# Optimization experiments

Hardware: AMD Instinct MI355X
Metric: run time of the kernel (lower is better)

## Reference

```python
import jax, jax.numpy as jnp
import numpy as np

N_NODES = 100000
N_EDGES = 1600000
NEG_SLOPE = 0.2  # PyG GATConv default


def _glorot(key, shape):
    fan = sum(shape[:2]) if len(shape) > 1 else shape[0] * 2
    s = jnp.sqrt(6.0 / fan)
    return jax.random.uniform(key, shape, jnp.float32, -s, s)


def gat_layer(x, src, dst, edge_attr, W, a_src, a_dst, We, a_e, b, heads, out_ch, concat):
    """Faithful PyG GATConv (add_self_loops=True, fill_value='mean', edge_dim set)."""
    n = x.shape[0]
    # self-loop edge_attr = mean of incoming edge_attr per dst node (0 if none)
    deg = jax.ops.segment_sum(jnp.ones((src.shape[0],), edge_attr.dtype), dst, num_segments=n)
    loop_attr = jax.ops.segment_sum(edge_attr, dst, num_segments=n) / jnp.maximum(deg, 1.0)[:, None]
    loop = jnp.arange(n, dtype=src.dtype)
    src_f = jnp.concatenate([src, loop])
    dst_f = jnp.concatenate([dst, loop])
    ea = jnp.concatenate([edge_attr, loop_attr], axis=0)
    # node transform -> [n, H, C]
    h = (x @ W).reshape(n, heads, out_ch)
    al_src = jnp.sum(h * a_src, axis=-1)  # [n, H]
    al_dst = jnp.sum(h * a_dst, axis=-1)  # [n, H]
    e = (ea @ We).reshape(-1, heads, out_ch)
    al_e = jnp.sum(e * a_e, axis=-1)      # [Ef, H]
    alpha = jax.nn.leaky_relu(al_src[src_f] + al_dst[dst_f] + al_e, negative_slope=NEG_SLOPE)
    # segment softmax over destination nodes (every node has a self loop)
    m = jax.ops.segment_max(alpha, dst_f, num_segments=n)
    ex = jnp.exp(alpha - m[dst_f])
    den = jax.ops.segment_sum(ex, dst_f, num_segments=n)
    att = ex / den[dst_f]                 # [Ef, H]
    out = jax.ops.segment_sum(att[:, :, None] * h[src_f], dst_f, num_segments=n)  # [n, H, C]
    out = out.reshape(n, heads * out_ch) if concat else out.mean(axis=1)
    return out + b


def setup_inputs() -> dict:
    key = jax.random.key(0)
    ks = jax.random.split(key, 20)
    x = jax.random.normal(ks[0], (N_NODES, 5), jnp.float32)
    edge_index = jax.random.randint(ks[1], (2, N_EDGES), 0, N_NODES, jnp.int64)
    edge_attr = jax.random.normal(ks[2], (N_EDGES, 2), jnp.float32)
    # conv1: in=5, out=32, heads=4, concat -> 128
    p = {
        "W1": _glorot(ks[3], (5, 128)), "aS1": _glorot(ks[4], (4, 32)),
        "aD1": _glorot(ks[5], (4, 32)), "We1": _glorot(ks[6], (2, 128)),
        "aE1": _glorot(ks[7], (4, 32)), "b1": jnp.zeros((128,), jnp.float32),
        # conv2: in=128, out=32, heads=2, concat -> 64
        "W2": _glorot(ks[8], (128, 64)), "aS2": _glorot(ks[9], (2, 32)),
        "aD2": _glorot(ks[10], (2, 32)), "We2": _glorot(ks[11], (2, 64)),
        "aE2": _glorot(ks[12], (2, 32)), "b2": jnp.zeros((64,), jnp.float32),
        # conv3: in=64, out=1, heads=1, concat=False
        "W3": _glorot(ks[13], (64, 1)), "aS3": _glorot(ks[14], (1, 1)),
        "aD3": _glorot(ks[15], (1, 1)), "We3": _glorot(ks[16], (2, 1)),
        "aE3": _glorot(ks[17], (1, 1)), "b3": jnp.zeros((1,), jnp.float32),
    }
    return {"x": x, "edge_index": edge_index, "edge_attr": edge_attr, **p}


def reference(x, edge_index, edge_attr,
              W1, aS1, aD1, We1, aE1, b1,
              W2, aS2, aD2, We2, aE2, b2,
              W3, aS3, aD3, We3, aE3, b3):
    src, dst = edge_index[0], edge_index[1]
    h = gat_layer(x, src, dst, edge_attr, W1, aS1, aD1, We1, aE1, b1, 4, 32, True)
    h = jax.nn.elu(h)  # dropout is identity in eval
    h = gat_layer(h, src, dst, edge_attr, W2, aS2, aD2, We2, aE2, b2, 2, 32, True)
    h = jax.nn.elu(h)
    h = gat_layer(h, src, dst, edge_attr, W3, aS3, aD3, We3, aE3, b3, 1, 1, False)
    return jax.nn.sigmoid(h).squeeze(-1)  # [N]
```

## Files before the change

### kernel.cpp

```cpp
#include <hip/hip_runtime.h>
#include <math.h>

#define NN 100000
#define NE 1600000
#define NPB 256
#define NB 391
#define NCHUNK 256
#define CH ((NE + NCHUNK - 1) / NCHUNK)
#define LOG2E 1.44269504088896f

__device__ __forceinline__ float lrelu(float x) { return fmaxf(x, 0.2f * x); }
__device__ __forceinline__ float elu1(float x) { return x > 0.f ? x : (__expf(x) - 1.f); }
__device__ __forceinline__ float fexp2(float x) {
#if __has_builtin(__builtin_amdgcn_exp2f)
    return __builtin_amdgcn_exp2f(x);
#else
    return exp2f(x);
#endif
}
__device__ __forceinline__ unsigned bf16rne(float f) {
    unsigned u = __float_as_uint(f);
    return (u + 0x7FFFu + ((u >> 16) & 1u)) >> 16;
}
__device__ __forceinline__ float bf16lo(unsigned u) { return __uint_as_float(u << 16); }
__device__ __forceinline__ float bf16hi(unsigned u) {
    return __uint_as_float(u & 0xFFFF0000u);
}

__global__ void __launch_bounds__(256) k_binA0(const int* __restrict__ dst,
                                               int* __restrict__ bucket_cnt) {
    __shared__ int hist[NB];
    int t = threadIdx.x;
    for (int b = t; b < NB; b += 256) hist[b] = 0;
    __syncthreads();
    int c0 = blockIdx.x * CH, c1 = min(NE, c0 + CH);
    for (int e = c0 + t; e < c1; e += 256) atomicAdd(&hist[dst[e] >> 8], 1);
    __syncthreads();
    for (int b = t; b < NB; b += 256)
        if (hist[b]) atomicAdd(&bucket_cnt[b], hist[b]);
}

__global__ void k_bscan(const int* __restrict__ bucket_cnt, int* __restrict__ bucket_base,
                        int* __restrict__ bucket_tail) {
    __shared__ int s[512];
    int t = threadIdx.x;
    int v = (t < NB) ? bucket_cnt[t] : 0;
    s[t] = v;
    __syncthreads();
    for (int off = 1; off < 512; off <<= 1) {
        int x = (t >= off) ? s[t - off] : 0;
        __syncthreads();
        if (t >= off) s[t] += x;
        __syncthreads();
    }
    if (t < NB) {
        int ex = s[t] - v;
        bucket_base[t] = ex;
        bucket_tail[t] = ex;
        if (t == NB - 1) bucket_base[NB] = s[t];
    }
}

__global__ void __launch_bounds__(256) k_binA2(const int* __restrict__ src,
                                               const int* __restrict__ dst,
                                               const float* __restrict__ ea,
                                               int* __restrict__ bucket_tail,
                                               uint2* __restrict__ binned,
                                               unsigned char* __restrict__ dstb) {
    __shared__ int hist[NB], base_l[NB], cursor[NB];
    int t = threadIdx.x;
    for (int b = t; b < NB; b += 256) {
        hist[b] = 0;
        cursor[b] = 0;
    }
    __syncthreads();
    int c0 = blockIdx.x * CH, c1 = min(NE, c0 + CH);
    for (int e = c0 + t; e < c1; e += 256) atomicAdd(&hist[dst[e] >> 8], 1);
    __syncthreads();
    for (int b = t; b < NB; b += 256)
        if (hist[b]) base_l[b] = atomicAdd(&bucket_tail[b], hist[b]);
    __syncthreads();
    for (int e = c0 + t; e < c1; e += 256) {
        int d = dst[e];
        int bkt = d >> 8;
        int idx = atomicAdd(&cursor[bkt], 1);
        int pos = base_l[bkt] + idx;
        unsigned pk = bf16rne(ea[2 * e]) | (bf16rne(ea[2 * e + 1]) << 16);
        binned[pos] = make_uint2((unsigned)src[e], pk);
        dstb[pos] = (unsigned char)(d & 255);
    }
}

__global__ void __launch_bounds__(256) k_binB(const int* __restrict__ bucket_base,
                                              const uint2* __restrict__ binned,
                                              const unsigned char* __restrict__ dstb,
                                              int* __restrict__ rowptr,
                                              uint2* __restrict__ edges) {
    __shared__ int hist[NPB], pre[NPB], cursor[NPB];
    int b = blockIdx.x, t = threadIdx.x;
    int bb = bucket_base[b], be = bucket_base[b + 1];
    int nb0 = b << 8;
    hist[t] = 0;
    __syncthreads();
    for (int e = bb + t; e < be; e += 256) atomicAdd(&hist[dstb[e]], 1);
    __syncthreads();
    int v = hist[t];
    pre[t] = v;
    __syncthreads();
    for (int off = 1; off < 256; off <<= 1) {
        int x = (t >= off) ? pre[t - off] : 0;
        __syncthreads();
        if (t >= off) pre[t] += x;
        __syncthreads();
    }
    int ex = pre[t] - v;
    if (nb0 + t <= NN) rowptr[nb0 + t] = bb + ex;
    cursor[t] = bb + ex;
    __syncthreads();
    for (int e = bb + t; e < be; e += 256) {
        uint2 rec = binned[e];
        int pos = atomicAdd(&cursor[dstb[e]], 1);
        edges[pos] = rec;
    }
}

__global__ void k_la(const int* __restrict__ rowptr, const uint2* __restrict__ edges,
                     float* __restrict__ la) {
    int n = (blockIdx.x * blockDim.x + threadIdx.x) >> 6;
    if (n >= NN) return;
    int lane = threadIdx.x & 63;
    int s0 = rowptr[n], e0 = rowptr[n + 1];
    float a0 = 0.f, a1 = 0.f;
    for (int e = s0 + lane; e < e0; e += 64) {
        unsigned pk = edges[e].y;
        a0 += bf16lo(pk);
        a1 += bf16hi(pk);
    }
#pragma unroll
    for (int off = 32; off > 0; off >>= 1) {
        a0 += __shfl_xor(a0, off);
        a1 += __shfl_xor(a1, off);
    }
    if (lane == 0) {
        float d = fmaxf((float)(e0 - s0), 1.0f);
        la[2 * n] = a0 / d;
        la[2 * n + 1] = a1 / d;
    }
}

template <int H, int C>
__global__ void k_me(const float* __restrict__ We, const float* __restrict__ aE,
                     float* __restrict__ me) {
    int t = threadIdx.x;
    if (t >= 2 * H) return;
    int d = t / H, hd = t % H;
    float s = 0.f;
    for (int c = 0; c < C; c++) s += We[d * H * C + hd * C + c] * aE[hd * C + c];
    me[t] = s * LOG2E;
}

__global__ void k_vsd(const float* __restrict__ W1, const float* __restrict__ aS1,
                      const float* __restrict__ aD1, float* __restrict__ vsd) {
    int t = threadIdx.x;
    if (t >= 40) return;
    const float* a = (t < 20) ? aS1 : aD1;
    int r = t % 20, hd = r / 5, i = r % 5;
    float s = 0.f;
    for (int c = 0; c < 32; c++) s += W1[i * 128 + hd * 32 + c] * a[hd * 32 + c];
    vsd[t] = s * LOG2E;
}

__global__ void k_prep1(const float* __restrict__ x, const float* __restrict__ vsd,
                        float4* __restrict__ xp, float4* __restrict__ als1,
                        float4* __restrict__ ald1) {
    int n = blockIdx.x * blockDim.x + threadIdx.x;
    if (n >= NN) return;
    float x0 = x[5 * n], x1 = x[5 * n + 1], x2 = x[5 * n + 2], x3 = x[5 * n + 3],
          x4 = x[5 * n + 4];
    xp[2 * n] = make_float4(x0, x1, x2, x3);
    xp[2 * n + 1] = make_float4(x4, 0.f, 0.f, 0.f);
    float sv[4], dv[4];
#pragma unroll
    for (int hd = 0; hd < 4; hd++) {
        const float* vS = vsd + hd * 5;
        const float* vD = vsd + 20 + hd * 5;
        sv[hd] = x0 * vS[0] + x1 * vS[1] + x2 * vS[2] + x3 * vS[3] + x4 * vS[4];
        dv[hd] = x0 * vD[0] + x1 * vD[1] + x2 * vD[2] + x3 * vD[3] + x4 * vD[4];
    }
    als1[n] = make_float4(sv[0], sv[1], sv[2], sv[3]);
    ald1[n] = make_float4(dv[0], dv[1], dv[2], dv[3]);
}

__global__ void k_agg1(const int* __restrict__ rowptr, const uint2* __restrict__ edges,
                       const float4* __restrict__ xp, const float* __restrict__ als1,
                       const float* __restrict__ ald1, const float* __restrict__ la,
                       const float* __restrict__ me, float* __restrict__ xw) {
    int t = blockIdx.x * blockDim.x + threadIdx.x;
    if (t >= NN * 4) return;
    int n = t >> 2, hd = t & 3;
    float me0 = me[hd], me1 = me[4 + hd];
    float aldn = ald1[t];
    float aself = lrelu(als1[t] + aldn + la[2 * n] * me0 + la[2 * n + 1] * me1);
    int start = rowptr[n], end = rowptr[n + 1];
    float den = 1.f;
    float4 xa = xp[2 * n];
    float xb = xp[2 * n + 1].x;
    float a0 = xa.x, a1 = xa.y, a2 = xa.z, a3 = xa.w, a4 = xb;
    for (int e = start; e < end; ++e) {
        uint2 ep = edges[e];
        int s = (int)ep.x;
        float a = lrelu(als1[s * 4 + hd] + aldn + bf16lo(ep.y) * me0 + bf16hi(ep.y) * me1);
        float p = fexp2(a - aself);
        den += p;
        float4 sa = xp[2 * s];
        float sb = xp[2 * s + 1].x;
        a0 += p * sa.x;
        a1 += p * sa.y;
        a2 += p * sa.z;
        a3 += p * sa.w;
        a4 += p * sb;
    }
    float r = 1.f / den;
    float* w = xw + (size_t)n * 20 + hd * 5;
    w[0] = a0 * r;
    w[1] = a1 * r;
    w[2] = a2 * r;
    w[3] = a3 * r;
    w[4] = a4 * r;
}

__global__ void __launch_bounds__(256) k_l2trans(
        const float* __restrict__ xw, const float* __restrict__ W1,
        const float* __restrict__ b1, const float* __restrict__ W2,
        const float* __restrict__ aS2, const float* __restrict__ aD2,
        unsigned short* __restrict__ h2q, float* __restrict__ als2,
        float* __restrict__ ald2) {
    __shared__ float sx[64 * 132];
    int nb = blockIdx.x * 64, t = threadIdx.x;
    {
        int nl = t >> 2, q = t & 3;
        int node = nb + nl;
        float w[20];
        if (node < NN) {
#pragma unroll
            for (int i = 0; i < 20; i++) w[i] = xw[(size_t)node * 20 + i];
        } else {
#pragma unroll
            for (int i = 0; i < 20; i++) w[i] = 0.f;
        }
#pragma unroll
        for (int k = 0; k < 32; k++) {
            int ch = q + 4 * k;
            int hd = ch >> 5;
            float v = w[hd * 5] * W1[ch] + w[hd * 5 + 1] * W1[128 + ch] +
                      w[hd * 5 + 2] * W1[256 + ch] + w[hd * 5 + 3] * W1[384 + ch] +
                      w[hd * 5 + 4] * W1[512 + ch] + b1[ch];
            sx[nl * 132 + ch] = (node < NN) ? elu1(v) : 0.f;
        }
    }
    __syncthreads();
    int jq = t & 15, ng = t >> 4;
    int j4 = jq * 4;
    float4 acc[4];
#pragma unroll
    for (int p = 0; p < 4; p++) acc[p] = make_float4(0.f, 0.f, 0.f, 0.f);
    for (int ic = 0; ic < 128; ic += 4) {
        float4 s[4];
#pragma unroll
        for (int p = 0; p < 4; p++)
            s[p] = *(const float4*)(sx + (ng * 4 + p) * 132 + ic);
#pragma unroll
        for (int r = 0; r < 4; r++) {
            float4 wv = *(const float4*)(W2 + (ic + r) * 64 + j4);
#pragma unroll
            for (int p = 0; p < 4; p++) {
                float sv = (r == 0) ? s[p].x : (r == 1) ? s[p].y : (r == 2) ? s[p].z : s[p].w;
                acc[p].x += sv * wv.x;
                acc[p].y += sv * wv.y;
                acc[p].z += sv * wv.z;
                acc[p].w += sv * wv.w;
            }
        }
    }
    int hd = jq >> 3;
    float4 a_s = *(const float4*)(aS2 + j4);
    float4 a_d = *(const float4*)(aD2 + j4);
    float pS[4], pD[4];
#pragma unroll
    for (int p = 0; p < 4; p++) {
        pS[p] = acc[p].x * a_s.x + acc[p].y * a_s.y + acc[p].z * a_s.z + acc[p].w * a_s.w;
        pD[p] = acc[p].x * a_d.x + acc[p].y * a_d.y + acc[p].z * a_d.z + acc[p].w * a_d.w;
    }
#pragma unroll
    for (int off = 1; off < 8; off <<= 1) {
#pragma unroll
        for (int p = 0; p < 4; p++) {
            pS[p] += __shfl_xor(pS[p], off);
            pD[p] += __shfl_xor(pD[p], off);
        }
    }
#pragma unroll
    for (int p = 0; p < 4; p++) {
        int node = nb + ng * 4 + p;
        if (node < NN) {
            ushort4 q;
            q.x = (unsigned short)bf16rne(acc[p].x);
            q.y = (unsigned short)bf16rne(acc[p].y);
            q.z = (unsigned short)bf16rne(acc[p].z);
            q.w = (unsigned short)bf16rne(acc[p].w);
            *(ushort4*)(h2q + (size_t)node * 64 + j4) = q;
            if ((jq & 7) == 0) {
                als2[node * 2 + hd] = pS[p] * LOG2E;
                ald2[node * 2 + hd] = pD[p] * LOG2E;
            }
        }
    }
}

__global__ void k_agg2(const int* __restrict__ rowptr, const uint2* __restrict__ edges,
                       const unsigned short* __restrict__ h2q,
                       const float* __restrict__ als2, const float* __restrict__ ald2,
                       const float* __restrict__ la, const float* __restrict__ me,
                       const float* __restrict__ b2, const float* __restrict__ W3,
                       float* __restrict__ h3) {
    int t = blockIdx.x * blockDim.x + threadIdx.x;
    if (t >= NN * 4) return;
    int n = t >> 2, sub = t & 3, hd = sub >> 1, qh = sub & 1;
    int cbase = hd * 32 + qh * 16;
    float me0 = me[hd], me1 = me[2 + hd];
    float aldn = ald2[n * 2 + hd];
    float aself = lrelu(als2[n * 2 + hd] + aldn + la[2 * n] * me0 + la[2 * n + 1] * me1);
    int start = rowptr[n], end = rowptr[n + 1];
    float den = 1.f;
    float acc[16];
    {
        const uint4* hp = (const uint4*)(h2q + (size_t)n * 64 + cbase);
        uint4 u0 = hp[0], u1 = hp[1];
        acc[0] = bf16lo(u0.x); acc[1] = bf16hi(u0.x);
        acc[2] = bf16lo(u0.y); acc[3] = bf16hi(u0.y);
        acc[4] = bf16lo(u0.z); acc[5] = bf16hi(u0.z);
        acc[6] = bf16lo(u0.w); acc[7] = bf16hi(u0.w);
        acc[8] = bf16lo(u1.x); acc[9] = bf16hi(u1.x);
        acc[10] = bf16lo(u1.y); acc[11] = bf16hi(u1.y);
        acc[12] = bf16lo(u1.z); acc[13] = bf16hi(u1.z);
        acc[14] = bf16lo(u1.w); acc[15] = bf16hi(u1.w);
    }
    for (int e = start; e < end; ++e) {
        uint2 ep = edges[e];
        int s = (int)ep.x;
        float a = lrelu(als2[s * 2 + hd] + aldn + bf16lo(ep.y) * me0 + bf16hi(ep.y) * me1);
        float p = fexp2(a - aself);
        den += p;
        const uint4* sp = (const uint4*)(h2q + (size_t)s * 64 + cbase);
        uint4 u0 = sp[0], u1 = sp[1];
        acc[0] += p * bf16lo(u0.x); acc[1] += p * bf16hi(u0.x);
        acc[2] += p * bf16lo(u0.y); acc[3] += p * bf16hi(u0.y);
        acc[4] += p * bf16lo(u0.z); acc[5] += p * bf16hi(u0.z);
        acc[6] += p * bf16lo(u0.w); acc[7] += p * bf16hi(u0.w);
        acc[8] += p * bf16lo(u1.x); acc[9] += p * bf16hi(u1.x);
        acc[10] += p * bf16lo(u1.y); acc[11] += p * bf16hi(u1.y);
        acc[12] += p * bf16lo(u1.z); acc[13] += p * bf16hi(u1.z);
        acc[14] += p * bf16lo(u1.w); acc[15] += p * bf16hi(u1.w);
    }
    float r = 1.f / den;
    float part = 0.f;
#pragma unroll
    for (int c = 0; c < 16; c++) {
        float v = elu1(acc[c] * r + b2[cbase + c]);
        part += v * W3[cbase + c];
    }
    part += __shfl_xor(part, 1);
    part += __shfl_xor(part, 2);
    if (sub == 0) h3[n] = part;
}

__global__ void k_agg3(const int* __restrict__ rowptr, const uint2* __restrict__ edges,
                       const float* __restrict__ h, const float* __restrict__ aS3,
                       const float* __restrict__ aD3, const float* __restrict__ la,
                       const float* __restrict__ me, const float* __restrict__ b,
                       float* __restrict__ out) {
    int n = (blockIdx.x * blockDim.x + threadIdx.x) >> 6;
    if (n >= NN) return;
    int lane = threadIdx.x & 63;
    float me0 = me[0], me1 = me[1];
    float aSs = aS3[0] * LOG2E, aDs = aD3[0] * LOG2E;
    float hn = h[n];
    float ald_n = hn * aDs;
    float aself = lrelu(hn * aSs + ald_n + la[2 * n] * me0 + la[2 * n + 1] * me1);
    int start = rowptr[n], end = rowptr[n + 1];
    float den = 0.f, num = 0.f;
    for (int e = start + lane; e < end; e += 64) {
        uint2 ep = edges[e];
        int s = (int)ep.x;
        float hv = h[s];
        float a = lrelu(hv * aSs + ald_n + bf16lo(ep.y) * me0 + bf16hi(ep.y) * me1);
        float p = fexp2(a - aself);
        den += p;
        num += p * hv;
    }
#pragma unroll
    for (int off = 32; off > 0; off >>= 1) {
        den += __shfl_xor(den, off);
        num += __shfl_xor(num, off);
    }
    if (lane == 0) {
        den += 1.f;
        num += hn;
        float v = num / den + b[0];
        out[n] = 1.f / (1.f + __expf(-v));
    }
}

extern "C" void kernel_launch(void* const* d_in, const int* in_sizes, int n_in,
                              void* d_out, int out_size, void* d_ws, size_t ws_size,
                              hipStream_t stream) {
    const float* x   = (const float*)d_in[0];
    const int*   ei  = (const int*)d_in[1];
    const float* ea  = (const float*)d_in[2];
    const float* W1  = (const float*)d_in[3];
    const float* aS1 = (const float*)d_in[4];
    const float* aD1 = (const float*)d_in[5];
    const float* We1 = (const float*)d_in[6];
    const float* aE1 = (const float*)d_in[7];
    const float* b1  = (const float*)d_in[8];
    const float* W2  = (const float*)d_in[9];
    const float* aS2 = (const float*)d_in[10];
    const float* aD2 = (const float*)d_in[11];
    const float* We2 = (const float*)d_in[12];
    const float* aE2 = (const float*)d_in[13];
    const float* b2  = (const float*)d_in[14];
    const float* W3  = (const float*)d_in[15];
    const float* aS3 = (const float*)d_in[16];
    const float* aD3 = (const float*)d_in[17];
    const float* We3 = (const float*)d_in[18];
    const float* aE3 = (const float*)d_in[19];
    const float* b3  = (const float*)d_in[20];

    const int* srcv = ei;
    const int* dstv = ei + NE;

    char* basep = (char*)d_ws;
    size_t off = 0;
    auto alloc = [&](size_t nbytes) -> void* {
        void* p = basep + off;
        off += (nbytes + 255) & ~(size_t)255;
        return p;
    };
    int*    bucket_cnt  = (int*)alloc((size_t)(NB + 1) * 4);
    int*    bucket_base = (int*)alloc((size_t)(NB + 1) * 4);
    int*    bucket_tail = (int*)alloc((size_t)(NB + 1) * 4);
    int*    rowptr      = (int*)alloc((size_t)(NN + 1) * 4);
    uint2*  binned      = (uint2*)alloc((size_t)NE * 8);
    unsigned char* dstb = (unsigned char*)alloc((size_t)NE);
    uint2*  edges       = (uint2*)alloc((size_t)NE * 8);
    float*  la          = (float*)alloc((size_t)NN * 8);
    float*  me          = (float*)alloc(256);
    float*  vsd         = (float*)alloc(256);
    float4* xp          = (float4*)alloc((size_t)NN * 32);
    float4* als1        = (float4*)alloc((size_t)NN * 16);
    float4* ald1        = (float4*)alloc((size_t)NN * 16);
    float*  xw          = (float*)alloc((size_t)NN * 80);
    unsigned short* h2q = (unsigned short*)alloc((size_t)NN * 128);
    float*  als2        = (float*)alloc((size_t)NN * 8);
    float*  ald2        = (float*)alloc((size_t)NN * 8);
    float*  h3          = (float*)alloc((size_t)NN * 4);
    (void)ws_size; (void)in_sizes; (void)n_in; (void)out_size;

    auto cdiv = [](long long a, long long b) { return (int)((a + b - 1) / b); };
    const int BS = 256;

    hipMemsetAsync(bucket_cnt, 0, (size_t)(NB + 1) * 4, stream);
    k_binA0<<<NCHUNK, 256, 0, stream>>>(dstv, bucket_cnt);
    k_bscan<<<1, 512, 0, stream>>>(bucket_cnt, bucket_base, bucket_tail);
    k_binA2<<<NCHUNK, 256, 0, stream>>>(srcv, dstv, ea, bucket_tail, binned, dstb);
    k_binB<<<NB, 256, 0, stream>>>(bucket_base, binned, dstb, rowptr, edges);
    k_la<<<cdiv(NN, 4), 256, 0, stream>>>(rowptr, edges, la);

    k_me<4, 32><<<1, 64, 0, stream>>>(We1, aE1, me);
    k_vsd<<<1, 64, 0, stream>>>(W1, aS1, aD1, vsd);
    k_prep1<<<cdiv(NN, BS), BS, 0, stream>>>(x, vsd, xp, als1, ald1);
    k_agg1<<<cdiv((long long)NN * 4, BS), BS, 0, stream>>>(rowptr, edges, xp,
                                                           (const float*)als1,
                                                           (const float*)ald1, la, me, xw);

    k_l2trans<<<cdiv(NN, 64), 256, 0, stream>>>(xw, W1, b1, W2, aS2, aD2, h2q, als2, ald2);
    k_me<2, 32><<<1, 64, 0, stream>>>(We2, aE2, me);
    k_agg2<<<cdiv((long long)NN * 4, BS), BS, 0, stream>>>(rowptr, edges, h2q, als2, ald2,
                                                           la, me, b2, W3, h3);

    k_me<1, 1><<<1, 64, 0, stream>>>(We3, aE3, me);
    k_agg3<<<cdiv(NN, 4), 256, 0, stream>>>(rowptr, edges, h3, aS3, aD3, la, me,
                                            b3, (float*)d_out);
}
```

Before: 360.6 us.

## Fuse self-loop attr mean into binning, merge constant kernels, shrink l2trans tile

The per-node mean of incoming edge attributes is now accumulated with shared-memory float atomics inside the bucket scatter kernel, which removes the separate k_la pass over the edge array. The four tiny constant-precompute kernels are merged into one launch that writes into a single buffer, cutting launch count. The layer-2 transform block now handles 32 nodes instead of 64, doubling the grid and halving shared memory and registers per block to raise occupancy. The price is shared float atomic contention in binB and a changed accumulation order for the mean.

```diff
diff --git a/kernel.cpp b/kernel.cpp
--- a/kernel.cpp
+++ b/kernel.cpp
@@ -95,12 +95,16 @@
                                               const uint2* __restrict__ binned,
                                               const unsigned char* __restrict__ dstb,
                                               int* __restrict__ rowptr,
-                                              uint2* __restrict__ edges) {
+                                              uint2* __restrict__ edges,
+                                              float* __restrict__ la) {
     __shared__ int hist[NPB], pre[NPB], cursor[NPB];
+    __shared__ float ea0s[NPB], ea1s[NPB];
     int b = blockIdx.x, t = threadIdx.x;
     int bb = bucket_base[b], be = bucket_base[b + 1];
     int nb0 = b << 8;
     hist[t] = 0;
+    ea0s[t] = 0.f;
+    ea1s[t] = 0.f;
     __syncthreads();
     for (int e = bb + t; e < be; e += 256) atomicAdd(&hist[dstb[e]], 1);
     __syncthreads();
@@ -119,55 +123,46 @@
     __syncthreads();
     for (int e = bb + t; e < be; e += 256) {
         uint2 rec = binned[e];
-        int pos = atomicAdd(&cursor[dstb[e]], 1);
+        unsigned char d = dstb[e];
+        int pos = atomicAdd(&cursor[d], 1);
         edges[pos] = rec;
-    }
-}
-
-__global__ void k_la(const int* __restrict__ rowptr, const uint2* __restrict__ edges,
-                     float* __restrict__ la) {
-    int n = (blockIdx.x * blockDim.x + threadIdx.x) >> 6;
-    if (n >= NN) return;
-    int lane = threadIdx.x & 63;
-    int s0 = rowptr[n], e0 = rowptr[n + 1];
-    float a0 = 0.f, a1 = 0.f;
-    for (int e = s0 + lane; e < e0; e += 64) {
-        unsigned pk = edges[e].y;
-        a0 += bf16lo(pk);
-        a1 += bf16hi(pk);
-    }
-#pragma unroll
-    for (int off = 32; off > 0; off >>= 1) {
-        a0 += __shfl_xor(a0, off);
-        a1 += __shfl_xor(a1, off);
-    }
-    if (lane == 0) {
-        float d = fmaxf((float)(e0 - s0), 1.0f);
-        la[2 * n] = a0 / d;
-        la[2 * n + 1] = a1 / d;
-    }
-}
-
-template <int H, int C>
-__global__ void k_me(const float* __restrict__ We, const float* __restrict__ aE,
-                     float* __restrict__ me) {
+        atomicAdd(&ea0s[d], bf16lo(rec.y));
+        atomicAdd(&ea1s[d], bf16hi(rec.y));
+    }
+    __syncthreads();
+    int n = nb0 + t;
+    if (n < NN) {
+        float dg = fmaxf((float)v, 1.0f);
+        la[2 * n] = ea0s[t] / dg;
+        la[2 * n + 1] = ea1s[t] / dg;
+    }
+}
+
+__global__ void k_const(const float* __restrict__ We1, const float* __restrict__ aE1,
+                        const float* __restrict__ We2, const float* __restrict__ aE2,
+                        const float* __restrict__ We3, const float* __restrict__ aE3,
+                        const float* __restrict__ W1, const float* __restrict__ aS1,
+                        const float* __restrict__ aD1, float* __restrict__ cbuf) {
     int t = threadIdx.x;
-    if (t >= 2 * H) return;
-    int d = t / H, hd = t % H;
-    float s = 0.f;
-    for (int c = 0; c < C; c++) s += We[d * H * C + hd * C + c] * aE[hd * C + c];
-    me[t] = s * LOG2E;
-}
-
-__global__ void k_vsd(const float* __restrict__ W1, const float* __restrict__ aS1,
-                      const float* __restrict__ aD1, float* __restrict__ vsd) {
-    int t = threadIdx.x;
-    if (t >= 40) return;
-    const float* a = (t < 20) ? aS1 : aD1;
-    int r = t % 20, hd = r / 5, i = r % 5;
-    float s = 0.f;
-    for (int c = 0; c < 32; c++) s += W1[i * 128 + hd * 32 + c] * a[hd * 32 + c];
-    vsd[t] = s * LOG2E;
+    if (t < 8) {
+        int d = t >> 2, hd = t & 3;
+        float s = 0.f;
+        for (int c = 0; c < 32; c++) s += We1[d * 128 + hd * 32 + c] * aE1[hd * 32 + c];
+        cbuf[t] = s * LOG2E;
+    } else if (t < 12) {
+        int idx = t - 8, d = idx >> 1, hd = idx & 1;
+        float s = 0.f;
+        for (int c = 0; c < 32; c++) s += We2[d * 64 + hd * 32 + c] * aE2[hd * 32 + c];
+        cbuf[t] = s * LOG2E;
+    } else if (t < 14) {
+        cbuf[t] = We3[t - 12] * aE3[0] * LOG2E;
+    } else if (t >= 16 && t < 56) {
+        int r = (t - 16) % 20, hd = r / 5, i = r % 5;
+        const float* a = (t - 16 < 20) ? aS1 : aD1;
+        float s = 0.f;
+        for (int c = 0; c < 32; c++) s += W1[i * 128 + hd * 32 + c] * a[hd * 32 + c];
+        cbuf[t] = s * LOG2E;
+    }
 }
 
 __global__ void k_prep1(const float* __restrict__ x, const float* __restrict__ vsd,
@@ -235,10 +230,10 @@
         const float* __restrict__ aS2, const float* __restrict__ aD2,
         unsigned short* __restrict__ h2q, float* __restrict__ als2,
         float* __restrict__ ald2) {
-    __shared__ float sx[64 * 132];
-    int nb = blockIdx.x * 64, t = threadIdx.x;
+    __shared__ float sx[32 * 132];
+    int nb = blockIdx.x * 32, t = threadIdx.x;
     {
-        int nl = t >> 2, q = t & 3;
+        int nl = t >> 3, q = t & 7;
         int node = nb + nl;
         float w[20];
         if (node < NN) {
@@ -249,8 +244,8 @@
             for (int i = 0; i < 20; i++) w[i] = 0.f;
         }
 #pragma unroll
-        for (int k = 0; k < 32; k++) {
-            int ch = q + 4 * k;
+        for (int k = 0; k < 16; k++) {
+            int ch = q + 8 * k;
             int hd = ch >> 5;
             float v = w[hd * 5] * W1[ch] + w[hd * 5 + 1] * W1[128 + ch] +
                       w[hd * 5 + 2] * W1[256 + ch] + w[hd * 5 + 3] * W1[384 + ch] +
@@ -261,19 +256,19 @@
     __syncthreads();
     int jq = t & 15, ng = t >> 4;
     int j4 = jq * 4;
-    float4 acc[4];
-#pragma unroll
-    for (int p = 0; p < 4; p++) acc[p] = make_float4(0.f, 0.f, 0.f, 0.f);
+    float4 acc[2];
+#pragma unroll
+    for (int p = 0; p < 2; p++) acc[p] = make_float4(0.f, 0.f, 0.f, 0.f);
     for (int ic = 0; ic < 128; ic += 4) {
-        float4 s[4];
-#pragma unroll
-        for (int p = 0; p < 4; p++)
-            s[p] = *(const float4*)(sx + (ng * 4 + p) * 132 + ic);
+        float4 s[2];
+#pragma unroll
+        for (int p = 0; p < 2; p++)
+            s[p] = *(const float4*)(sx + (ng * 2 + p) * 132 + ic);
 #pragma unroll
         for (int r = 0; r < 4; r++) {
             float4 wv = *(const float4*)(W2 + (ic + r) * 64 + j4);
 #pragma unroll
-            for (int p = 0; p < 4; p++) {
+            for (int p = 0; p < 2; p++) {
                 float sv = (r == 0) ? s[p].x : (r == 1) ? s[p].y : (r == 2) ? s[p].z : s[p].w;
                 acc[p].x += sv * wv.x;
                 acc[p].y += sv * wv.y;
@@ -285,23 +280,23 @@
     int hd = jq >> 3;
     float4 a_s = *(const float4*)(aS2 + j4);
     float4 a_d = *(const float4*)(aD2 + j4);
-    float pS[4], pD[4];
-#pragma unroll
-    for (int p = 0; p < 4; p++) {
+    float pS[2], pD[2];
+#pragma unroll
+    for (int p = 0; p < 2; p++) {
         pS[p] = acc[p].x * a_s.x + acc[p].y * a_s.y + acc[p].z * a_s.z + acc[p].w * a_s.w;
         pD[p] = acc[p].x * a_d.x + acc[p].y * a_d.y + acc[p].z * a_d.z + acc[p].w * a_d.w;
     }
 #pragma unroll
     for (int off = 1; off < 8; off <<= 1) {
 #pragma unroll
-        for (int p = 0; p < 4; p++) {
+        for (int p = 0; p < 2; p++) {
             pS[p] += __shfl_xor(pS[p], off);
             pD[p] += __shfl_xor(pD[p], off);
         }
     }
 #pragma unroll
-    for (int p = 0; p < 4; p++) {
-        int node = nb + ng * 4 + p;
+    for (int p = 0; p < 2; p++) {
+        int node = nb + ng * 2 + p;
         if (node < NN) {
             ushort4 q;
             q.x = (unsigned short)bf16rne(acc[p].x);
@@ -454,8 +449,7 @@
     unsigned char* dstb = (unsigned char*)alloc((size_t)NE);
     uint2*  edges       = (uint2*)alloc((size_t)NE * 8);
     float*  la          = (float*)alloc((size_t)NN * 8);
-    float*  me          = (float*)alloc(256);
-    float*  vsd         = (float*)alloc(256);
+    float*  cbuf        = (float*)alloc(256);
     float4* xp          = (float4*)alloc((size_t)NN * 32);
     float4* als1        = (float4*)alloc((size_t)NN * 16);
     float4* ald1        = (float4*)alloc((size_t)NN * 16);
@@ -466,6 +460,11 @@
     float*  h3          = (float*)alloc((size_t)NN * 4);
     (void)ws_size; (void)in_sizes; (void)n_in; (void)out_size;
 
+    float* me1 = cbuf;
+    float* me2 = cbuf + 8;
+    float* me3 = cbuf + 12;
+    float* vsd = cbuf + 16;
+
     auto cdiv = [](long long a, long long b) { return (int)((a + b - 1) / b); };
     const int BS = 256;
 
@@ -473,22 +472,19 @@
     k_binA0<<<NCHUNK, 256, 0, stream>>>(dstv, bucket_cnt);
     k_bscan<<<1, 512, 0, stream>>>(bucket_cnt, bucket_base, bucket_tail);
     k_binA2<<<NCHUNK, 256, 0, stream>>>(srcv, dstv, ea, bucket_tail, binned, dstb);
-    k_binB<<<NB, 256, 0, stream>>>(bucket_base, binned, dstb, rowptr, edges);
-    k_la<<<cdiv(NN, 4), 256, 0, stream>>>(rowptr, edges, la);
-
-    k_me<4, 32><<<1, 64, 0, stream>>>(We1, aE1, me);
-    k_vsd<<<1, 64, 0, stream>>>(W1, aS1, aD1, vsd);
+    k_binB<<<NB, 256, 0, stream>>>(bucket_base, binned, dstb, rowptr, edges, la);
+
+    k_const<<<1, 64, 0, stream>>>(We1, aE1, We2, aE2, We3, aE3, W1, aS1, aD1, cbuf);
+
     k_prep1<<<cdiv(NN, BS), BS, 0, stream>>>(x, vsd, xp, als1, ald1);
     k_agg1<<<cdiv((long long)NN * 4, BS), BS, 0, stream>>>(rowptr, edges, xp,
                                                            (const float*)als1,
-                                                           (const float*)ald1, la, me, xw);
-
-    k_l2trans<<<cdiv(NN, 64), 256, 0, stream>>>(xw, W1, b1, W2, aS2, aD2, h2q, als2, ald2);
-    k_me<2, 32><<<1, 64, 0, stream>>>(We2, aE2, me);
+                                                           (const float*)ald1, la, me1, xw);
+
+    k_l2trans<<<cdiv(NN, 32), 256, 0, stream>>>(xw, W1, b1, W2, aS2, aD2, h2q, als2, ald2);
     k_agg2<<<cdiv((long long)NN * 4, BS), BS, 0, stream>>>(rowptr, edges, h2q, als2, ald2,
-                                                           la, me, b2, W3, h3);
-
-    k_me<1, 1><<<1, 64, 0, stream>>>(We3, aE3, me);
-    k_agg3<<<cdiv(NN, 4), 256, 0, stream>>>(rowptr, edges, h3, aS3, aD3, la, me,
+                                                           la, me2, b2, W3, h3);
+
+    k_agg3<<<cdiv(NN, 4), 256, 0, stream>>>(rowptr, edges, h3, aS3, aD3, la, me3,
                                             b3, (float*)d_out);
 }
```

After: 377.8 us. 4.8% more time.
